# Optimization experiments

Measured on AMD Instinct MI355X. Metric: run time of the kernel, lower is better.

## Reference

```python
import jax, jax.numpy as jnp
import numpy as np

IN_CH = 64
OUT_CH = 64
SEQ_LEN = 2048
MODES = 64  # modes2 = min(modes1, seq_len//2) = 64
SCALE = 1.0 / (IN_CH * OUT_CH)


def setup_inputs() -> dict:
    key = jax.random.key(0)
    k1, k2, k3 = jax.random.split(key, 3)
    x = jax.random.normal(k1, (32, 8, IN_CH, SEQ_LEN), dtype=jnp.float32)
    # torch.rand(...) complex init scaled by 1/(in*out): real & imag in [0, scale)
    wr = SCALE * jax.random.uniform(k2, (IN_CH, OUT_CH, MODES), dtype=jnp.float32)
    wi = SCALE * jax.random.uniform(k3, (IN_CH, OUT_CH, MODES), dtype=jnp.float32)
    return {"x": x, "wr": wr, "wi": wi}


def reference(x, wr, wi):
    # x: [B, H, E, N] real; weights complex [in, out, modes]
    N = x.shape[-1]
    w = jax.lax.complex(wr, wi)
    x_ft = jnp.fft.rfft(x)                       # [B, H, E, N//2+1] complex64
    a = x_ft[..., :MODES]                        # keep only low modes
    out_low = jnp.einsum('bjix,iox->bjox', a, w)  # per-mode complex matmul
    # zero-fill remaining frequency bins (equivalent to out_ft zeros + slice set)
    pad = N // 2 + 1 - MODES
    out_ft = jnp.pad(out_low, ((0, 0), (0, 0), (0, 0), (0, pad)))
    return jnp.fft.irfft(out_ft, n=N)            # [B, H, out_ch, N] real
```

## Files before the change

kernel.cpp:

```cpp
#include <hip/hip_runtime.h>
#include <hip/hip_bf16.h>


typedef __bf16 bf16x8 __attribute__((ext_vector_type(8)));
typedef float  f32x4  __attribute__((ext_vector_type(4)));

#define SEQ 2048
#define NM2 128
#define KS  2

__device__ __forceinline__ unsigned int rnbf(float f) {
  unsigned int u = __builtin_bit_cast(unsigned int, f);
  return (u + 0x7fffu + ((u >> 16) & 1u)) >> 16;
}
__device__ __forceinline__ unsigned int pack2(float a, float b) {
  return rnbf(a) | (rnbf(b) << 16);
}
__device__ __forceinline__ float frombf(unsigned int lo16_in_place) {
  return __builtin_bit_cast(float, lo16_in_place);
}

typedef const __attribute__((address_space(1))) unsigned int gu32;
typedef __attribute__((address_space(3))) unsigned int lu32;

__global__ __launch_bounds__(256) void k_tables(unsigned short* __restrict__ t1sw,
                                                unsigned short* __restrict__ t2sw) {
  int idx = blockIdx.x * 256 + threadIdx.x;
  int k = idx >> 11;
  int n = idx & 2047;
  float rev = (float)((k * n) & 2047) * (1.0f / 2048.0f);
  float s, co;
  asm("v_sin_f32 %0, %1" : "=v"(s)  : "v"(rev));
  asm("v_cos_f32 %0, %1" : "=v"(co) : "v"(rev));
  float ck = (k == 0 ? 1.0f : 2.0f) * (1.0f / 2048.0f);
  {
    int kt = n >> 6, part = (n >> 3) & 7, e = n & 7;
    unsigned base = (unsigned)kt * 16384u + 2u * (unsigned)e;
    unsigned offc = base + (((unsigned)(k * 128 + part * 16)) ^ (((unsigned)k & 7u) << 4));
    int c2 = k + 64;
    unsigned offs = base + (((unsigned)(c2 * 128 + part * 16)) ^ (((unsigned)c2 & 7u) << 4));
    *(unsigned short*)((char*)t1sw + offc) = (unsigned short)rnbf(co);
    *(unsigned short*)((char*)t1sw + offs) = (unsigned short)rnbf(-s);
  }
  {
    int tile = n >> 7, rl = n & 127;
    unsigned rowbase = (unsigned)tile * 32768u + (unsigned)rl * 128u;
    unsigned kpart = ((((unsigned)(k >> 3)) * 16u) ^ (((unsigned)rl & 7u) << 4)) + 2u * ((unsigned)k & 7u);
    *(unsigned short*)((char*)t2sw + rowbase + kpart)          = (unsigned short)rnbf(ck * co);
    *(unsigned short*)((char*)t2sw + rowbase + 16384u + kpart) = (unsigned short)rnbf(-ck * s);
  }
}

__global__ __launch_bounds__(256) void k_gemm1(const float* __restrict__ x,
                                               const unsigned short* __restrict__ t1sw,
                                               unsigned short* __restrict__ P) {
  __shared__ int4 lds4[65536 / 16];
  char* lds = (char*)lds4;
  const int tid = threadIdx.x, wave = tid >> 6, lane = tid & 63;
  const int mtile = blockIdx.x >> 1, ks = blockIdx.x & (KS - 1);
  const int r0 = mtile * 64;
  const int kbase = ks * (SEQ / KS);
  const char* t1base = (const char*)t1sw + (size_t)(kbase >> 6) * 16384;

  const float* xsrc[4];
#pragma unroll
  for (int p = 0; p < 4; ++p) {
    const int row = p * 16 + wave * 4 + (lane >> 4);
    const int u = (lane & 15) ^ (row & 7);
    xsrc[p] = x + (size_t)(r0 + row) * SEQ + kbase + u * 4;
  }

  f32x4 acc[8] = {};

#pragma unroll
  for (int p = 0; p < 4; ++p)
    __builtin_amdgcn_global_load_lds((gu32*)(xsrc[p]),
                                     (lu32*)(lds + p * 4096 + wave * 1024), 16, 0, 0);
#pragma unroll
  for (int p = 0; p < 4; ++p)
    __builtin_amdgcn_global_load_lds((gu32*)(t1base + (p * 256 + tid) * 16),
                                     (lu32*)(lds + 32768 + (p * 256 + wave * 64) * 16), 16, 0, 0);
  asm volatile("s_waitcnt vmcnt(0)" ::: "memory");
  __builtin_amdgcn_s_barrier();

  const int a = wave * 16 + (lane & 15);
  const unsigned xra = (unsigned)(a & 7) << 4;
  const int kg = lane >> 4;

  for (int it = 0; it < 16; ++it) {
    const int cur = it & 1, nxt = cur ^ 1;
    const int xoff = cur * 16384;
    const int toff = 32768 + cur * 16384;
    if (it < 15) {
      const char* tg = t1base + (size_t)(it + 1) * 16384;
#pragma unroll
      for (int p = 0; p < 4; ++p)
        __builtin_amdgcn_global_load_lds((gu32*)(xsrc[p] + (it + 1) * 64),
                                         (lu32*)(lds + nxt * 16384 + p * 4096 + wave * 1024),
                                         16, 0, 0);
#pragma unroll
      for (int p = 0; p < 4; ++p)
        __builtin_amdgcn_global_load_lds((gu32*)(tg + (p * 256 + tid) * 16),
                                         (lu32*)(lds + 32768 + nxt * 16384 + (p * 256 + wave * 64) * 16),
                                         16, 0, 0);
    }
#pragma unroll
    for (int kss = 0; kss < 2; ++kss) {
      const unsigned byte0 = (unsigned)(a * 256 + kss * 128 + kg * 32);
      const f32x4 lo = *(const f32x4*)(lds + xoff + (byte0 ^ xra));
      const f32x4 hi = *(const f32x4*)(lds + xoff + ((byte0 + 16) ^ xra));
      unsigned c0, c1, c2, c3;
      asm("v_cvt_pk_bf16_f32 %0, %1, %2" : "=v"(c0) : "v"(lo[0]), "v"(lo[1]));
      asm("v_cvt_pk_bf16_f32 %0, %1, %2" : "=v"(c1) : "v"(lo[2]), "v"(lo[3]));
      asm("v_cvt_pk_bf16_f32 %0, %1, %2" : "=v"(c2) : "v"(hi[0]), "v"(hi[1]));
      asm("v_cvt_pk_bf16_f32 %0, %1, %2" : "=v"(c3) : "v"(hi[2]), "v"(hi[3]));
      uint4 pk; pk.x = c0; pk.y = c1; pk.z = c2; pk.w = c3;
      const bf16x8 av = __builtin_bit_cast(bf16x8, pk);
#pragma unroll
      for (int t = 0; t < 8; ++t) {
        const int col = t * 16 + (lane & 15);
        const bf16x8 bv = *(const bf16x8*)(lds + toff +
            ((col * 128 + kss * 64 + kg * 16) ^ ((unsigned)(col & 7) << 4)));
        acc[t] = __builtin_amdgcn_mfma_f32_16x16x32_bf16(bv, av, acc[t], 0, 0, 0);
      }
    }
    asm volatile("s_waitcnt vmcnt(0)" ::: "memory");
    __builtin_amdgcn_s_barrier();
  }
  unsigned short* Pout = P + (size_t)ks * (16384 * NM2);
  const int row = r0 + wave * 16 + (lane & 15);
#pragma unroll
  for (int t = 0; t < 8; ++t) {
    const int col0 = t * 16 + kg * 4;
    uint2 v; v.x = pack2(acc[t][0], acc[t][1]); v.y = pack2(acc[t][2], acc[t][3]);
    *(uint2*)(Pout + (size_t)row * NM2 + col0) = v;
  }
}

__global__ __launch_bounds__(256) void k_stage2(const unsigned short* __restrict__ P,
                                                const float* __restrict__ wr,
                                                const float* __restrict__ wi,
                                                char* __restrict__ Bxsw) {
  __shared__ float sA[4][64][64];
  const int b = blockIdx.x;
  const int bjc = b >> 2, oh = (b >> 1) & 1, kh = b & 1;
  const int k0 = kh * 32;
  const int tid = threadIdx.x;
#pragma unroll
  for (int p = 0; p < 16; ++p) {
    int fidx = tid + 256 * p;
    int row_lin = fidx >> 4, q = fidx & 15;
    int col = (q < 8) ? (k0 + q * 4) : (64 + k0 + (q - 8) * 4);
    const unsigned short* base = P + (size_t)(bjc * 256 + row_lin) * NM2 + col;
    f32x4 v = {};
#pragma unroll
    for (int s = 0; s < KS; ++s) {
      uint2 u = *(const uint2*)(base + (size_t)s * (16384 * NM2));
      v[0] += frombf(u.x << 16);
      v[1] += frombf(u.x & 0xffff0000u);
      v[2] += frombf(u.y << 16);
      v[3] += frombf(u.y & 0xffff0000u);
    }
    *(f32x4*)(&sA[row_lin >> 6][row_lin & 63][q * 4]) = v;
  }
  __syncthreads();
  const int o_l = tid >> 3, kg = tid & 7;
  const int o = oh * 32 + o_l;
  const int kb = k0 + kg * 4;
  f32x4 accr[4] = {};
  f32x4 acci[4] = {};
  for (int i = 0; i < 64; ++i) {
    f32x4 wrv = *(const f32x4*)(wr + (i * 64 + o) * 64 + kb);
    f32x4 wiv = *(const f32x4*)(wi + (i * 64 + o) * 64 + kb);
#pragma unroll
    for (int bj = 0; bj < 4; ++bj) {
      f32x4 ar = *(const f32x4*)(&sA[bj][i][kg * 4]);
      f32x4 ai = *(const f32x4*)(&sA[bj][i][32 + kg * 4]);
#pragma unroll
      for (int kk = 0; kk < 4; ++kk) {
        accr[bj][kk] += ar[kk] * wrv[kk] - ai[kk] * wiv[kk];
        acci[bj][kk] += ar[kk] * wiv[kk] + ai[kk] * wrv[kk];
      }
    }
  }
#pragma unroll
  for (int bj = 0; bj < 4; ++bj) {
    const int r = (bjc * 4 + bj) * 64 + o;
    const int tile = r >> 7, rl = r & 127;
    char* bb = Bxsw + (size_t)tile * 32768 + (size_t)rl * 128;
    const unsigned kp = ((((unsigned)kb >> 3) * 16u) ^ (((unsigned)rl & 7u) << 4)) + 2u * ((unsigned)kb & 7u);
    uint2 vr; vr.x = pack2(accr[bj][0], accr[bj][1]); vr.y = pack2(accr[bj][2], accr[bj][3]);
    uint2 vi; vi.x = pack2(acci[bj][0], acci[bj][1]); vi.y = pack2(acci[bj][2], acci[bj][3]);
    *(uint2*)(bb + kp)          = vr;
    *(uint2*)(bb + 16384 + kp)  = vi;
  }
}

__global__ __launch_bounds__(256) void k_gemm2(const char* __restrict__ Bxsw,
                                               const char* __restrict__ t2sw,
                                               float* __restrict__ out) {
  __shared__ int4 lds4[49152 / 16];
  char* lds = (char*)lds4;
  const int tid = threadIdx.x, wave = tid >> 6, lane = tid & 63;
  const int swz = (blockIdx.x & 7) * 512 + (blockIdx.x >> 3);
  const int mb = swz >> 5, nb64 = swz & 31;
  const int r0 = mb * 128, n0 = nb64 * 64;
  const char* bsrc = Bxsw + (size_t)mb * 32768;
  const char* tsrc = t2sw + (size_t)(nb64 >> 1) * 32768 + (size_t)(nb64 & 1) * 8192;
#pragma unroll
  for (int i = 0; i < 4; ++i)
    __builtin_amdgcn_global_load_lds((gu32*)(bsrc + i * 4096 + tid * 16),
                                     (lu32*)(lds + i * 4096 + wave * 1024), 16, 0, 0);
#pragma unroll
  for (int i = 0; i < 2; ++i)
    __builtin_amdgcn_global_load_lds((gu32*)(tsrc + i * 4096 + tid * 16),
                                     (lu32*)(lds + 32768 + i * 4096 + wave * 1024), 16, 0, 0);
#pragma unroll
  for (int i = 0; i < 4; ++i)
    __builtin_amdgcn_global_load_lds((gu32*)(bsrc + 16384 + i * 4096 + tid * 16),
                                     (lu32*)(lds + 16384 + i * 4096 + wave * 1024), 16, 0, 0);
#pragma unroll
  for (int i = 0; i < 2; ++i)
    __builtin_amdgcn_global_load_lds((gu32*)(tsrc + 16384 + i * 4096 + tid * 16),
                                     (lu32*)(lds + 40960 + i * 4096 + wave * 1024), 16, 0, 0);
  asm volatile("s_waitcnt vmcnt(6)" ::: "memory");
  __builtin_amdgcn_s_barrier();

  f32x4 acc[2][4] = {};
  const int rowA0 = wave * 32 + (lane & 15);
  const int rowA1 = rowA0 + 16;
  const unsigned xa0 = (unsigned)(rowA0 & 7) << 4;
  const unsigned xa1 = (unsigned)(rowA1 & 7) << 4;

#pragma unroll
  for (int half = 0; half < 2; ++half) {
    if (half == 1) {
      asm volatile("s_waitcnt vmcnt(0)" ::: "memory");
      __builtin_amdgcn_s_barrier();
    }
    const int ab = half * 16384;
    const int bb = 32768 + half * 8192;
#pragma unroll
    for (int kq = 0; kq < 2; ++kq) {
      const unsigned offh = (unsigned)(kq * 64 + (lane >> 4) * 16);
      const bf16x8 a0 = *(const bf16x8*)(lds + ab + rowA0 * 128 + (offh ^ xa0));
      const bf16x8 a1 = *(const bf16x8*)(lds + ab + rowA1 * 128 + (offh ^ xa1));
#pragma unroll
      for (int t = 0; t < 4; ++t) {
        const int rn = t * 16 + (lane & 15);
        const bf16x8 bv = *(const bf16x8*)(lds + bb + rn * 128 + (offh ^ ((unsigned)(rn & 7) << 4)));
        acc[0][t] = __builtin_amdgcn_mfma_f32_16x16x32_bf16(a0, bv, acc[0][t], 0, 0, 0);
        acc[1][t] = __builtin_amdgcn_mfma_f32_16x16x32_bf16(a1, bv, acc[1][t], 0, 0, 0);
      }
    }
  }
#pragma unroll
  for (int m = 0; m < 2; ++m) {
#pragma unroll
    for (int j = 0; j < 4; ++j) {
      const int row = r0 + wave * 32 + m * 16 + (lane >> 4) * 4 + j;
#pragma unroll
      for (int t = 0; t < 4; ++t) {
        const int col = n0 + t * 16 + (lane & 15);
        out[(size_t)row * SEQ + col] = acc[m][t][j];
      }
    }
  }
}

extern "C" void kernel_launch(void* const* d_in, const int* in_sizes, int n_in,
                              void* d_out, int out_size, void* d_ws, size_t ws_size,
                              hipStream_t stream) {
  const float* x  = (const float*)d_in[0];
  const float* wr = (const float*)d_in[1];
  const float* wi = (const float*)d_in[2];
  float* out = (float*)d_out;
  char* ws = (char*)d_ws;
  unsigned short* t1sw = (unsigned short*)(ws);
  unsigned short* t2sw = (unsigned short*)(ws + 524288);
  unsigned short* P    = (unsigned short*)(ws + 1048576);
  char*           Bxsw = (char*)(ws + 1048576 + (size_t)KS * 16384 * NM2 * 2);

  k_tables<<<dim3(512),      dim3(256), 0, stream>>>(t1sw, t2sw);
  k_gemm1 <<<dim3(256 * KS), dim3(256), 0, stream>>>(x, t1sw, P);
  k_stage2<<<dim3(256),      dim3(256), 0, stream>>>(P, wr, wi, Bxsw);
  k_gemm2 <<<dim3(4096),     dim3(256), 0, stream>>>(Bxsw, (const char*)t2sw, out);
}
```

Baseline: 88.59 us.

## Fuse forward DFT GEMM with per-mode complex weight contraction, drop split-K

Merges the forward DFT GEMM and the per-mode channel mixing into a single kernel. Each block of 512 threads now covers a full 64-row (bj) slice over the whole sequence instead of splitting K in two. The fp32 spectrum is staged in LDS and contracted with the complex weights in place. This removes the bf16 partial-sum buffer round trip and one kernel launch. In exchange the grid drops to 256 blocks with a longer serial K loop, which may reduce parallelism and latency hiding.

```diff
diff --git a/kernel.cpp b/kernel.cpp
--- a/kernel.cpp
+++ b/kernel.cpp
@@ -7,7 +7,6 @@
 
 #define SEQ 2048
 #define NM2 128
-#define KS  2
 
 __device__ __forceinline__ unsigned int rnbf(float f) {
   unsigned int u = __builtin_bit_cast(unsigned int, f);
@@ -15,9 +14,6 @@
 }
 __device__ __forceinline__ unsigned int pack2(float a, float b) {
   return rnbf(a) | (rnbf(b) << 16);
-}
-__device__ __forceinline__ float frombf(unsigned int lo16_in_place) {
-  return __builtin_bit_cast(float, lo16_in_place);
 }
 
 typedef const __attribute__((address_space(1))) unsigned int gu32;
@@ -51,58 +47,60 @@
   }
 }
 
-__global__ __launch_bounds__(256) void k_gemm1(const float* __restrict__ x,
-                                               const unsigned short* __restrict__ t1sw,
-                                               unsigned short* __restrict__ P) {
+__global__ __launch_bounds__(512) void k_gemm1f(const float* __restrict__ x,
+                                                const unsigned short* __restrict__ t1sw,
+                                                const float* __restrict__ wre,
+                                                const float* __restrict__ wim,
+                                                char* __restrict__ Bxsw) {
   __shared__ int4 lds4[65536 / 16];
   char* lds = (char*)lds4;
   const int tid = threadIdx.x, wave = tid >> 6, lane = tid & 63;
-  const int mtile = blockIdx.x >> 1, ks = blockIdx.x & (KS - 1);
-  const int r0 = mtile * 64;
-  const int kbase = ks * (SEQ / KS);
-  const char* t1base = (const char*)t1sw + (size_t)(kbase >> 6) * 16384;
-
-  const float* xsrc[4];
-#pragma unroll
-  for (int p = 0; p < 4; ++p) {
-    const int row = p * 16 + wave * 4 + (lane >> 4);
+  const int bj = blockIdx.x;
+  const int r0 = bj * 64;
+
+  const float* xsrc[2];
+#pragma unroll
+  for (int p = 0; p < 2; ++p) {
+    const int row = p * 32 + wave * 4 + (lane >> 4);
     const int u = (lane & 15) ^ (row & 7);
-    xsrc[p] = x + (size_t)(r0 + row) * SEQ + kbase + u * 4;
-  }
-
-  f32x4 acc[8] = {};
-
-#pragma unroll
-  for (int p = 0; p < 4; ++p)
-    __builtin_amdgcn_global_load_lds((gu32*)(xsrc[p]),
-                                     (lu32*)(lds + p * 4096 + wave * 1024), 16, 0, 0);
-#pragma unroll
-  for (int p = 0; p < 4; ++p)
-    __builtin_amdgcn_global_load_lds((gu32*)(t1base + (p * 256 + tid) * 16),
-                                     (lu32*)(lds + 32768 + (p * 256 + wave * 64) * 16), 16, 0, 0);
+    xsrc[p] = x + (size_t)(r0 + row) * SEQ + u * 4;
+  }
+
+  f32x4 acc[4] = {};
+
+#define XSTAGE(it, buf)                                                               \
+  {                                                                                   \
+    _Pragma("unroll")                                                                 \
+    for (int p = 0; p < 2; ++p)                                                       \
+      __builtin_amdgcn_global_load_lds((gu32*)(xsrc[p] + (it) * 64),                  \
+          (lu32*)(lds + (buf) * 16384 + p * 8192 + wave * 1024), 16, 0, 0);           \
+  }
+#define TSTAGE(it, buf)                                                               \
+  {                                                                                   \
+    const char* tg_ = (const char*)t1sw + (size_t)(it) * 16384;                       \
+    _Pragma("unroll")                                                                 \
+    for (int q = 0; q < 2; ++q)                                                       \
+      __builtin_amdgcn_global_load_lds((gu32*)(tg_ + (q * 512 + tid) * 16),           \
+          (lu32*)(lds + 32768 + (buf) * 16384 + q * 8192 + wave * 1024), 16, 0, 0);   \
+  }
+
+  XSTAGE(0, 0);
+  TSTAGE(0, 0);
   asm volatile("s_waitcnt vmcnt(0)" ::: "memory");
   __builtin_amdgcn_s_barrier();
 
-  const int a = wave * 16 + (lane & 15);
+  const int wr4 = wave >> 1, wc = wave & 1;
+  const int a = wr4 * 16 + (lane & 15);
   const unsigned xra = (unsigned)(a & 7) << 4;
   const int kg = lane >> 4;
 
-  for (int it = 0; it < 16; ++it) {
+  for (int it = 0; it < 32; ++it) {
     const int cur = it & 1, nxt = cur ^ 1;
     const int xoff = cur * 16384;
     const int toff = 32768 + cur * 16384;
-    if (it < 15) {
-      const char* tg = t1base + (size_t)(it + 1) * 16384;
-#pragma unroll
-      for (int p = 0; p < 4; ++p)
-        __builtin_amdgcn_global_load_lds((gu32*)(xsrc[p] + (it + 1) * 64),
-                                         (lu32*)(lds + nxt * 16384 + p * 4096 + wave * 1024),
-                                         16, 0, 0);
-#pragma unroll
-      for (int p = 0; p < 4; ++p)
-        __builtin_amdgcn_global_load_lds((gu32*)(tg + (p * 256 + tid) * 16),
-                                         (lu32*)(lds + 32768 + nxt * 16384 + (p * 256 + wave * 64) * 16),
-                                         16, 0, 0);
+    if (it < 31) {
+      XSTAGE(it + 1, nxt);
+      TSTAGE(it + 1, nxt);
     }
 #pragma unroll
     for (int kss = 0; kss < 2; ++kss) {
@@ -117,8 +115,8 @@
       uint4 pk; pk.x = c0; pk.y = c1; pk.z = c2; pk.w = c3;
       const bf16x8 av = __builtin_bit_cast(bf16x8, pk);
 #pragma unroll
-      for (int t = 0; t < 8; ++t) {
-        const int col = t * 16 + (lane & 15);
+      for (int t = 0; t < 4; ++t) {
+        const int col = wc * 64 + t * 16 + (lane & 15);
         const bf16x8 bv = *(const bf16x8*)(lds + toff +
             ((col * 128 + kss * 64 + kg * 16) ^ ((unsigned)(col & 7) << 4)));
         acc[t] = __builtin_amdgcn_mfma_f32_16x16x32_bf16(bv, av, acc[t], 0, 0, 0);
@@ -127,73 +125,46 @@
     asm volatile("s_waitcnt vmcnt(0)" ::: "memory");
     __builtin_amdgcn_s_barrier();
   }
-  unsigned short* Pout = P + (size_t)ks * (16384 * NM2);
-  const int row = r0 + wave * 16 + (lane & 15);
-#pragma unroll
-  for (int t = 0; t < 8; ++t) {
-    const int col0 = t * 16 + kg * 4;
-    uint2 v; v.x = pack2(acc[t][0], acc[t][1]); v.y = pack2(acc[t][2], acc[t][3]);
-    *(uint2*)(Pout + (size_t)row * NM2 + col0) = v;
-  }
-}
-
-__global__ __launch_bounds__(256) void k_stage2(const unsigned short* __restrict__ P,
-                                                const float* __restrict__ wr,
-                                                const float* __restrict__ wi,
-                                                char* __restrict__ Bxsw) {
-  __shared__ float sA[4][64][64];
-  const int b = blockIdx.x;
-  const int bjc = b >> 2, oh = (b >> 1) & 1, kh = b & 1;
-  const int k0 = kh * 32;
-  const int tid = threadIdx.x;
-#pragma unroll
-  for (int p = 0; p < 16; ++p) {
-    int fidx = tid + 256 * p;
-    int row_lin = fidx >> 4, q = fidx & 15;
-    int col = (q < 8) ? (k0 + q * 4) : (64 + k0 + (q - 8) * 4);
-    const unsigned short* base = P + (size_t)(bjc * 256 + row_lin) * NM2 + col;
-    f32x4 v = {};
-#pragma unroll
-    for (int s = 0; s < KS; ++s) {
-      uint2 u = *(const uint2*)(base + (size_t)s * (16384 * NM2));
-      v[0] += frombf(u.x << 16);
-      v[1] += frombf(u.x & 0xffff0000u);
-      v[2] += frombf(u.y << 16);
-      v[3] += frombf(u.y & 0xffff0000u);
-    }
-    *(f32x4*)(&sA[row_lin >> 6][row_lin & 63][q * 4]) = v;
+#undef XSTAGE
+#undef TSTAGE
+
+  float* sA = (float*)lds;
+#pragma unroll
+  for (int t = 0; t < 4; ++t) {
+    const int col0 = wc * 64 + t * 16 + kg * 4;
+    *(f32x4*)(sA + a * 136 + col0) = acc[t];
   }
   __syncthreads();
-  const int o_l = tid >> 3, kg = tid & 7;
-  const int o = oh * 32 + o_l;
-  const int kb = k0 + kg * 4;
-  f32x4 accr[4] = {};
-  f32x4 acci[4] = {};
+
+  const int o = tid >> 3;
+  const int kb = (tid & 7) * 8;
+  f32x4 accr0 = {}, accr1 = {}, acci0 = {}, acci1 = {};
   for (int i = 0; i < 64; ++i) {
-    f32x4 wrv = *(const f32x4*)(wr + (i * 64 + o) * 64 + kb);
-    f32x4 wiv = *(const f32x4*)(wi + (i * 64 + o) * 64 + kb);
-#pragma unroll
-    for (int bj = 0; bj < 4; ++bj) {
-      f32x4 ar = *(const f32x4*)(&sA[bj][i][kg * 4]);
-      f32x4 ai = *(const f32x4*)(&sA[bj][i][32 + kg * 4]);
-#pragma unroll
-      for (int kk = 0; kk < 4; ++kk) {
-        accr[bj][kk] += ar[kk] * wrv[kk] - ai[kk] * wiv[kk];
-        acci[bj][kk] += ar[kk] * wiv[kk] + ai[kk] * wrv[kk];
-      }
-    }
-  }
-#pragma unroll
-  for (int bj = 0; bj < 4; ++bj) {
-    const int r = (bjc * 4 + bj) * 64 + o;
-    const int tile = r >> 7, rl = r & 127;
-    char* bb = Bxsw + (size_t)tile * 32768 + (size_t)rl * 128;
-    const unsigned kp = ((((unsigned)kb >> 3) * 16u) ^ (((unsigned)rl & 7u) << 4)) + 2u * ((unsigned)kb & 7u);
-    uint2 vr; vr.x = pack2(accr[bj][0], accr[bj][1]); vr.y = pack2(accr[bj][2], accr[bj][3]);
-    uint2 vi; vi.x = pack2(acci[bj][0], acci[bj][1]); vi.y = pack2(acci[bj][2], acci[bj][3]);
-    *(uint2*)(bb + kp)          = vr;
-    *(uint2*)(bb + 16384 + kp)  = vi;
-  }
+    const float* wp = wre + (size_t)(i * 64 + o) * 64 + kb;
+    const float* wq = wim + (size_t)(i * 64 + o) * 64 + kb;
+    const f32x4 w0 = *(const f32x4*)(wp),     w1 = *(const f32x4*)(wp + 4);
+    const f32x4 v0 = *(const f32x4*)(wq),     v1 = *(const f32x4*)(wq + 4);
+    const float* ap = sA + i * 136 + kb;
+    const f32x4 ar0 = *(const f32x4*)(ap),      ar1 = *(const f32x4*)(ap + 4);
+    const f32x4 ai0 = *(const f32x4*)(ap + 64), ai1 = *(const f32x4*)(ap + 68);
+#pragma unroll
+    for (int kk = 0; kk < 4; ++kk) {
+      accr0[kk] += ar0[kk] * w0[kk] - ai0[kk] * v0[kk];
+      accr1[kk] += ar1[kk] * w1[kk] - ai1[kk] * v1[kk];
+      acci0[kk] += ar0[kk] * v0[kk] + ai0[kk] * w0[kk];
+      acci1[kk] += ar1[kk] * v1[kk] + ai1[kk] * w1[kk];
+    }
+  }
+  const int r = bj * 64 + o;
+  const int tile = r >> 7, rl = r & 127;
+  char* bb = Bxsw + (size_t)tile * 32768 + (size_t)rl * 128;
+  const unsigned kp0 = (((unsigned)(kb >> 3)) * 16u) ^ (((unsigned)rl & 7u) << 4);
+  uint4 vr; vr.x = pack2(accr0[0], accr0[1]); vr.y = pack2(accr0[2], accr0[3]);
+            vr.z = pack2(accr1[0], accr1[1]); vr.w = pack2(accr1[2], accr1[3]);
+  uint4 vi; vi.x = pack2(acci0[0], acci0[1]); vi.y = pack2(acci0[2], acci0[3]);
+            vi.z = pack2(acci1[0], acci1[1]); vi.w = pack2(acci1[2], acci1[3]);
+  *(uint4*)(bb + kp0)         = vr;
+  *(uint4*)(bb + 16384 + kp0) = vi;
 }
 
 __global__ __launch_bounds__(256) void k_gemm2(const char* __restrict__ Bxsw,
@@ -278,11 +249,9 @@
   char* ws = (char*)d_ws;
   unsigned short* t1sw = (unsigned short*)(ws);
   unsigned short* t2sw = (unsigned short*)(ws + 524288);
-  unsigned short* P    = (unsigned short*)(ws + 1048576);
-  char*           Bxsw = (char*)(ws + 1048576 + (size_t)KS * 16384 * NM2 * 2);
-
-  k_tables<<<dim3(512),      dim3(256), 0, stream>>>(t1sw, t2sw);
-  k_gemm1 <<<dim3(256 * KS), dim3(256), 0, stream>>>(x, t1sw, P);
-  k_stage2<<<dim3(256),      dim3(256), 0, stream>>>(P, wr, wi, Bxsw);
-  k_gemm2 <<<dim3(4096),     dim3(256), 0, stream>>>(Bxsw, (const char*)t2sw, out);
-}
+  char*           Bxsw = (char*)(ws + 1048576);
+
+  k_tables<<<dim3(512),  dim3(256), 0, stream>>>(t1sw, t2sw);
+  k_gemm1f<<<dim3(256),  dim3(512), 0, stream>>>(x, t1sw, wr, wi, Bxsw);
+  k_gemm2 <<<dim3(4096), dim3(256), 0, stream>>>(Bxsw, (const char*)t2sw, out);
+}
```

Result: no change. 89.76 us (+1.3%).
